# Kernel tuning notes

Hardware: AMD Instinct MI355X
Metric: run time of the kernel (lower is better)

## Reference

```python
import jax, jax.numpy as jnp
import numpy as np
from jax import lax

EPS = 1e-5

def haar_dwt(x):
    # pywt 'haar' dwt2: a=(x0+x1)/sqrt2, d=(x0-x1)/sqrt2 per axis
    B, C, H, W = x.shape
    xr = x.reshape(B, C, H // 2, 2, W // 2, 2)
    x00 = xr[:, :, :, 0, :, 0]; x01 = xr[:, :, :, 0, :, 1]
    x10 = xr[:, :, :, 1, :, 0]; x11 = xr[:, :, :, 1, :, 1]
    ll = (x00 + x01 + x10 + x11) * 0.5
    lh = (x00 + x01 - x10 - x11) * 0.5  # cH: detail along rows
    hl = (x00 - x01 + x10 - x11) * 0.5  # cV: detail along cols
    hh = (x00 - x01 - x10 + x11) * 0.5  # cD
    return ll, lh, hl, hh

def haar_idwt(ll, lh, hl, hh):
    y00 = (ll + lh + hl + hh) * 0.5
    y01 = (ll + lh - hl - hh) * 0.5
    y10 = (ll - lh + hl - hh) * 0.5
    y11 = (ll - lh - hl + hh) * 0.5
    B, C, H, W = ll.shape
    top = jnp.stack([y00, y01], axis=-1)      # [B,C,H,W,2]
    bot = jnp.stack([y10, y11], axis=-1)
    y = jnp.stack([top, bot], axis=3)          # [B,C,H,2,W,2]
    return y.reshape(B, C, 2 * H, 2 * W)

def conv1x1(x, w, b):
    # w: [Cout, Cin]
    return jnp.einsum('bchw,oc->bohw', x, w) + b[None, :, None, None]

def batchnorm(x, g, b):
    mu = jnp.mean(x, axis=(0, 2, 3), keepdims=True)
    var = jnp.var(x, axis=(0, 2, 3), keepdims=True)
    xh = (x - mu) * lax.rsqrt(var + EPS)
    return xh * g[None, :, None, None] + b[None, :, None, None]

def layernorm_chw(x, g, b):
    # GroupNorm(1, C): normalize over (C,H,W) per sample
    mu = jnp.mean(x, axis=(1, 2, 3), keepdims=True)
    var = jnp.var(x, axis=(1, 2, 3), keepdims=True)
    xh = (x - mu) * lax.rsqrt(var + EPS)
    return xh * g[None, :, None, None] + b[None, :, None, None]

def dwconv3x3(x, w, b):
    # w: [C,1,3,3] depthwise
    C = x.shape[1]
    y = lax.conv_general_dilated(x, w, (1, 1), [(1, 1), (1, 1)],
                                 dimension_numbers=('NCHW', 'OIHW', 'NCHW'),
                                 feature_group_count=C)
    return y + b[None, :, None, None]

gelu = lambda x: jax.nn.gelu(x, approximate=False)

def setup_inputs() -> dict:
    key = jax.random.key(0)
    ks = jax.random.split(key, 16)
    C = 128
    B, H, W = 8, 256, 256
    f = jnp.float32
    s = lambda k, shape, fan: jax.random.normal(k, shape, f) * (1.0 / np.sqrt(fan))
    return {
        'x': jax.random.normal(ks[0], (B, C, H, W), f),
        'w_c1': s(ks[1], (C, 4 * C), 4 * C), 'b_c1': jnp.zeros((C,), f),
        'bn1_g': jnp.ones((C,), f), 'bn1_b': jnp.zeros((C,), f),
        'dw_w': s(ks[2], (C, 1, 3, 3), 9), 'dw_b': jnp.zeros((C,), f),
        'gn_g': jnp.ones((C,), f), 'gn_b': jnp.zeros((C,), f),
        'pw1_w': s(ks[3], (C, C), C), 'pw1_b': jnp.zeros((C,), f),
        'pw2_w': s(ks[4], (C, C), C), 'pw2_b': jnp.zeros((C,), f),
        'w_c2': s(ks[5], (4 * C, C), C), 'b_c2': jnp.zeros((4 * C,), f),
        'bn2_g': jnp.ones((4 * C,), f), 'bn2_b': jnp.zeros((4 * C,), f),
    }

def reference(x, w_c1, b_c1, bn1_g, bn1_b, dw_w, dw_b, gn_g, gn_b,
              pw1_w, pw1_b, pw2_w, pw2_b, w_c2, b_c2, bn2_g, bn2_b):
    ll, lh, hl, hh = haar_dwt(x)
    h = jnp.concatenate([ll, lh, hl, hh], axis=1)       # [B,4C,H/2,W/2]
    h = gelu(batchnorm(conv1x1(h, w_c1, b_c1), bn1_g, bn1_b))
    # BasicBlock
    res = h
    o = dwconv3x3(h, dw_w, dw_b)
    o = layernorm_chw(o, gn_g, gn_b)
    o = conv1x1(o, pw1_w, pw1_b)
    o = gelu(o)
    o = conv1x1(o, pw2_w, pw2_b)
    h = o + res
    h = gelu(batchnorm(conv1x1(h, w_c2, b_c2), bn2_g, bn2_b))
    C = h.shape[1] // 4
    return haar_idwt(h[:, :C], h[:, C:2 * C], h[:, 2 * C:3 * C], h[:, 3 * C:])
```

## Files before the change

### kernel.cpp

```cpp
#include <hip/hip_runtime.h>
#include <hip/hip_bf16.h>

typedef unsigned short u16;
typedef unsigned int u32;
typedef __attribute__((ext_vector_type(8))) short short8;
typedef __attribute__((ext_vector_type(4))) float f32x4;

#define Bq 8
#define Cc 128
#define C4 512
#define Hh 256
#define Wf 256
#define H2 128
#define W2 128
#define HW2 16384
#define NPIX 131072.0f

__device__ __forceinline__ float gelu_f(float x) {
    float u = 1.5957691216057308f * (x + 0.044715f * x * x * x);
    float t = 1.0f - 2.0f / (__expf(u) + 1.0f);
    return 0.5f * x * (1.0f + t);
}
__device__ __forceinline__ float bf2f(u16 u) {
    union { float f; u32 i; } v; v.i = ((u32)u) << 16; return v.f;
}
__device__ __forceinline__ u16 f2bf(float f) {
    union { float f; u32 i; } v; v.f = f;
    u32 r = v.i + 0x7FFFu + ((v.i >> 16) & 1u);
    return (u16)(r >> 16);
}

__global__ __launch_bounds__(256) void k_wconv(const float* __restrict__ w_c1,
                                               const float* __restrict__ pw1,
                                               const float* __restrict__ pw2,
                                               const float* __restrict__ w_c2,
                                               const float* __restrict__ gn_g,
                                               u16* __restrict__ wb) {
    int i = blockIdx.x * 256 + threadIdx.x;
    float v;
    if (i < 65536) {
        int o = i >> 9, kn = i & 511;
        int c = kn >> 2, dy = (kn >> 1) & 1, dx = kn & 1;
        float sdy = dy ? -1.f : 1.f, sdx = dx ? -1.f : 1.f;
        const float* wr = w_c1 + o * 512 + c;
        v = 0.5f * (wr[0] + sdy * wr[128] + sdx * wr[256] + sdy * sdx * wr[384]);
    } else if (i < 81920) v = pw1[i - 65536] * gn_g[(i - 65536) & 127];
    else if (i < 98304) v = pw2[i - 81920];
    else v = w_c2[i - 98304];
    wb[i] = f2bf(v);
}

__global__ __launch_bounds__(128) void k_wvec(const float* __restrict__ pw1,
                                              const float* __restrict__ gg,
                                              const float* __restrict__ gb,
                                              float* __restrict__ wbv,
                                              float* __restrict__ wgs) {
    int o = threadIdx.x;
    float a = 0.f, bv = 0.f;
    for (int c = 0; c < 128; ++c) {
        float w = pw1[o * 128 + c];
        a += w * gg[c];
        bv += w * gb[c];
    }
    wgs[o] = a;
    wbv[o] = bv;
}

__global__ __launch_bounds__(512) void k_conv1(const float* __restrict__ x,
                                               const u16* __restrict__ Wt,
                                               u16* __restrict__ Cout,
                                               float* __restrict__ statS,
                                               float* __restrict__ statQ) {
    __shared__ __align__(16) u16 lds[16384];
    __shared__ float sblk[128], qblk[128];
    const int t = threadIdx.x;
    const int lane = t & 63, w = t >> 6, wr = w & 1, wc = w >> 1;
    const int b = blockIdx.z, i = blockIdx.y;
    if (t < 128) { sblk[t] = 0.f; qblk[t] = 0.f; }

    const int r15 = lane & 15, kq = lane >> 4;
    const int half = t >> 8;
    const int colblk = t & 7, cc = (t >> 3) & 15, dy = (t >> 7) & 1;
    const int kbase = cc * 4 + dy * 2;
    const int gG = kbase >> 3, e2 = (kbase & 7) * 2;

    float4 xv[4];
    uint4 rb[2];
    {
        const float* xp = x + (((long)(b * Cc + cc)) * Hh + (2 * i + dy)) * Wf;
#pragma unroll
        for (int q = 0; q < 4; ++q) {
            int col = (half * 4 + q) * 32 + colblk * 4;
            xv[q] = *(const float4*)(xp + col);
        }
#pragma unroll
        for (int ii = 0; ii < 2; ++ii) {
            int s = ii * 512 + t;
            rb[ii] = *(const uint4*)(Wt + (long)(s >> 3) * 512 + (s & 7) * 8);
        }
    }

    f32x4 acc[4][2];
#pragma unroll
    for (int a2 = 0; a2 < 4; ++a2)
#pragma unroll
        for (int j2 = 0; j2 < 2; ++j2) acc[a2][j2] = (f32x4){0.f, 0.f, 0.f, 0.f};

    for (int k0 = 0; k0 < 512; k0 += 64) {
        __syncthreads();
#pragma unroll
        for (int q = 0; q < 4; ++q) {
            int col = (half * 4 + q) * 32 + colblk * 4;
            int j0 = col >> 1;
            u32 p0 = (u32)f2bf(xv[q].x) | ((u32)f2bf(xv[q].y) << 16);
            u32 p1 = (u32)f2bf(xv[q].z) | ((u32)f2bf(xv[q].w) << 16);
            *(u32*)((char*)lds + j0 * 128 + 16 * (gG ^ (j0 & 7)) + e2) = p0;
            *(u32*)((char*)lds + (j0 + 1) * 128 + 16 * (gG ^ ((j0 + 1) & 7)) + e2) = p1;
        }
#pragma unroll
        for (int ii = 0; ii < 2; ++ii) {
            int s = ii * 512 + t;
            int row_ = s >> 3, ch_ = s & 7;
            *(uint4*)((char*)lds + 16384 + row_ * 128 + 16 * (ch_ ^ (row_ & 7))) = rb[ii];
        }
        __syncthreads();
        if (k0 + 64 < 512) {
            const int c0n = (k0 + 64) >> 2;
            const float* xp = x + (((long)(b * Cc + c0n + cc)) * Hh + (2 * i + dy)) * Wf;
#pragma unroll
            for (int q = 0; q < 4; ++q) {
                int col = (half * 4 + q) * 32 + colblk * 4;
                xv[q] = *(const float4*)(xp + col);
            }
#pragma unroll
            for (int ii = 0; ii < 2; ++ii) {
                int s = ii * 512 + t;
                rb[ii] = *(const uint4*)(Wt + (long)(s >> 3) * 512 + (k0 + 64) + (s & 7) * 8);
            }
        }
#pragma unroll
        for (int ks = 0; ks < 2; ++ks) {
            short8 af[4], bfv[2];
            const int ch = ks * 4 + kq;
#pragma unroll
            for (int mi = 0; mi < 4; ++mi) {
                int row = wr * 64 + mi * 16 + r15;
                af[mi] = *(const short8*)((const char*)lds + row * 128 + 16 * (ch ^ (row & 7)));
            }
#pragma unroll
            for (int ni = 0; ni < 2; ++ni) {
                int row = wc * 32 + ni * 16 + r15;
                bfv[ni] = *(const short8*)((const char*)lds + 16384 + row * 128 + 16 * (ch ^ (row & 7)));
            }
#pragma unroll
            for (int mi = 0; mi < 4; ++mi)
#pragma unroll
                for (int ni = 0; ni < 2; ++ni)
                    acc[mi][ni] = __builtin_amdgcn_mfma_f32_16x16x32_bf16(
                        af[mi], bfv[ni], acc[mi][ni], 0, 0, 0);
        }
    }
    __syncthreads();

#pragma unroll
    for (int mi = 0; mi < 4; ++mi)
#pragma unroll
        for (int ni = 0; ni < 2; ++ni)
#pragma unroll
            for (int r = 0; r < 4; ++r) {
                int row = wr * 64 + mi * 16 + kq * 4 + r;
                int col = wc * 32 + ni * 16 + r15;
                lds[row * 128 + (col ^ ((row & 7) << 3))] = f2bf(acc[mi][ni][r]);
            }
#pragma unroll
    for (int ni = 0; ni < 2; ++ni) {
        float s = 0.f, q2 = 0.f;
#pragma unroll
        for (int mi = 0; mi < 4; ++mi)
#pragma unroll
            for (int r = 0; r < 4; ++r) {
                float v = acc[mi][ni][r];
                s += v; q2 += v * v;
            }
        s += __shfl_down(s, 32); s += __shfl_down(s, 16);
        q2 += __shfl_down(q2, 32); q2 += __shfl_down(q2, 16);
        if (lane < 16) {
            int col = wc * 32 + ni * 16 + r15;
            atomicAdd(&sblk[col], s);
            atomicAdd(&qblk[col], q2);
        }
    }
    __syncthreads();
    {
        u16* Cb = Cout + (long)b * HW2 * 128;
        int row = t >> 2, quarter = (t & 3) * 32;
        int sx = (row & 7) << 3;
        long gbase = (long)(i * 128 + row) * 128;
#pragma unroll
        for (int q = 0; q < 4; ++q) {
            int c = quarter + q * 8;
            *(uint4*)(Cb + gbase + c) = *(const uint4*)(lds + row * 128 + (c ^ sx));
        }
    }
    if (t < 128) {
        atomicAdd(statS + (long)t * 16, sblk[t]);
        atomicAdd(statQ + (long)t * 16, qblk[t]);
    }
}

__global__ __launch_bounds__(256) void k_dwconv(const u16* __restrict__ xin,
                                                u16* __restrict__ y,
                                                const float* __restrict__ w,
                                                const float* __restrict__ bias,
                                                const float* __restrict__ bnS,
                                                const float* __restrict__ bnQ,
                                                const float* __restrict__ g1,
                                                const float* __restrict__ b1,
                                                float* __restrict__ lnS,
                                                float* __restrict__ lnQ) {
    __shared__ float wl2[1152];
    __shared__ float sA[128], sB[128];
    __shared__ __align__(16) u16 tile[3 * 18 * 136];
    const int t = threadIdx.x;
    if (t < 128) {
        const float invN = 1.0f / 131072.0f;
        float mu = bnS[(long)t * 16] * invN;
        float var = bnQ[(long)t * 16] * invN - mu * mu;
        float rs = rsqrtf(var + 1e-5f);
        float sc = rs * g1[t];
        sA[t] = sc;
        sB[t] = b1[t] - mu * sc;
    }
    for (int idx = t; idx < 1152; idx += 256) {
        int c = idx / 9, tap = idx - c * 9;
        wl2[tap * 128 + (c & 7) * 16 + (c >> 3)] = w[idx];
    }
    __syncthreads();
    const int jbase = blockIdx.x * 16, i = blockIdx.y, b = blockIdx.z;
    const u16* xb = xin + (long)b * HW2 * 128;
    {
        int seg = t & 15, slot0 = t >> 4;
#pragma unroll
        for (int pass = 0; pass < 4; ++pass) {
            int slot = pass * 16 + slot0;
            if (slot < 54) {
                int r = slot / 18, p = slot - r * 18;
                int row = i - 1 + r, col = jbase - 1 + p;
                bool inb = (row >= 0) & (row < H2) & (col >= 0) & (col < W2);
                uint4 raw = inb ? *(const uint4*)(xb + ((long)row * W2 + col) * 128 + seg * 8)
                                : make_uint4(0u, 0u, 0u, 0u);
                const u16* pv = (const u16*)&raw;
                uint4 outv; u16* ov = (u16*)&outv;
#pragma unroll
                for (int u = 0; u < 8; ++u) {
                    int c = seg * 8 + u;
                    float v = inb ? gelu_f(bf2f(pv[u]) * sA[c] + sB[c]) : 0.f;
                    ov[u] = f2bf(v);
                }
                *(uint4*)(tile + slot * 136 + seg * 8) = outv;
            }
        }
    }
    __syncthreads();
    const int cg = t & 15, jj = t >> 4;
    float acc[8];
#pragma unroll
    for (int u = 0; u < 8; ++u) acc[u] = bias[cg * 8 + u];
#pragma unroll
    for (int r = 0; r < 3; ++r)
#pragma unroll
        for (int dj = 0; dj < 3; ++dj) {
            short8 vv = *(const short8*)(tile + (r * 18 + jj + dj) * 136 + cg * 8);
            const int tap = r * 3 + dj;
#pragma unroll
            for (int u = 0; u < 8; ++u)
                acc[u] = fmaf(bf2f((u16)vv[u]), wl2[tap * 128 + u * 16 + cg], acc[u]);
        }
    uint4 outv; u16* ov = (u16*)&outv;
    float s = 0.f, q2 = 0.f;
#pragma unroll
    for (int u = 0; u < 8; ++u) {
        ov[u] = f2bf(acc[u]);
        s += acc[u]; q2 += acc[u] * acc[u];
    }
    *(uint4*)(y + ((long)b * HW2 + (long)i * W2 + jbase + jj) * 128 + cg * 8) = outv;
#pragma unroll
    for (int off = 32; off; off >>= 1) {
        s += __shfl_down(s, off);
        q2 += __shfl_down(q2, off);
    }
    __shared__ float r1[4], r2[4];
    if ((t & 63) == 0) { r1[t >> 6] = s; r2[t >> 6] = q2; }
    __syncthreads();
    if (t == 0) {
        int slot = (blockIdx.y * 8 + blockIdx.x) & 63;
        atomicAdd(lnS + ((long)b * 64 + slot) * 16, r1[0] + r1[1] + r1[2] + r1[3]);
        atomicAdd(lnQ + ((long)b * 64 + slot) * 16, r2[0] + r2[1] + r2[2] + r2[3]);
    }
}

__global__ __launch_bounds__(256) void k_mlp(const u16* __restrict__ D,
                                             const u16* __restrict__ Wp1,
                                             const u16* __restrict__ Wp2,
                                             const float* __restrict__ b1p,
                                             const float* __restrict__ b2p,
                                             const u16* __restrict__ resA,
                                             u16* __restrict__ Yout,
                                             const float* __restrict__ lnS,
                                             const float* __restrict__ lnQ,
                                             const float* __restrict__ wbv,
                                             const float* __restrict__ wgs,
                                             const float* __restrict__ bnS,
                                             const float* __restrict__ bnQ,
                                             const float* __restrict__ g1,
                                             const float* __restrict__ b1v) {
    __shared__ __align__(16) u16 lA[16384];
    __shared__ __align__(16) u16 lB[16384];
    __shared__ float s1[128], s2[128], sA[128], sB[128], lnred[2];
    const int t = threadIdx.x;
    const int lane = t & 63, w = t >> 6, wr = w >> 1, wc = w & 1;
    const int r15 = lane & 15, kq = lane >> 4;
    const int b = blockIdx.z, m0 = blockIdx.y * 128;

    if (t < 64) {
        float s = lnS[((long)b * 64 + t) * 16];
        float q = lnQ[((long)b * 64 + t) * 16];
#pragma unroll
        for (int off = 32; off; off >>= 1) {
            s += __shfl_down(s, off);
            q += __shfl_down(q, off);
        }
        if (t == 0) { lnred[0] = s; lnred[1] = q; }
    }
    __syncthreads();
    const float invN = 1.0f / 2097152.0f;
    float mu = lnred[0] * invN;
    float var = lnred[1] * invN - mu * mu;
    const float rs = rsqrtf(var + 1e-5f);
    if (t < 128) {
        s1[t] = b1p[t] + wbv[t] - mu * rs * wgs[t];
        s2[t] = b2p[t];
        const float invN1 = 1.0f / 131072.0f;
        float mu1 = bnS[(long)t * 16] * invN1;
        float var1 = bnQ[(long)t * 16] * invN1 - mu1 * mu1;
        float rs1 = rsqrtf(var1 + 1e-5f);
        float sc1 = rs1 * g1[t];
        sA[t] = sc1;
        sB[t] = b1v[t] - mu1 * sc1;
    }

    const u16* Ab = D + ((long)b * HW2 + m0) * 128;
    uint4 ga[8], gb[8];
#pragma unroll
    for (int i = 0; i < 8; ++i) {
        int s = i * 256 + t, row = s >> 4, seg = s & 15;
        ga[i] = *(const uint4*)(Ab + (long)row * 128 + seg * 8);
        gb[i] = *(const uint4*)(Wp1 + (long)row * 128 + seg * 8);
    }
#pragma unroll
    for (int i = 0; i < 8; ++i) {
        int s = i * 256 + t, row = s >> 4, seg = s & 15;
        int off = (seg >> 3) * 16384 + row * 128 + 16 * ((seg & 7) ^ (row & 7));
        *(uint4*)((char*)lA + off) = ga[i];
        *(uint4*)((char*)lB + off) = gb[i];
    }
    __syncthreads();

    f32x4 acc[4][4];
#pragma unroll
    for (int i = 0; i < 4; ++i)
#pragma unroll
        for (int j = 0; j < 4; ++j) acc[i][j] = (f32x4){0.f, 0.f, 0.f, 0.f};
#pragma unroll
    for (int chunk = 0; chunk < 2; ++chunk)
#pragma unroll
        for (int ks = 0; ks < 2; ++ks) {
            const int ch = ks * 4 + kq;
            short8 af[4], bfv[4];
#pragma unroll
            for (int mi = 0; mi < 4; ++mi) {
                int row = wr * 64 + mi * 16 + r15;
                af[mi] = *(const short8*)((const char*)lA + chunk * 16384 +
                                          row * 128 + 16 * (ch ^ (row & 7)));
            }
#pragma unroll
            for (int ni = 0; ni < 4; ++ni) {
                int row = wc * 64 + ni * 16 + r15;
                bfv[ni] = *(const short8*)((const char*)lB + chunk * 16384 +
                                           row * 128 + 16 * (ch ^ (row & 7)));
            }
#pragma unroll
            for (int mi = 0; mi < 4; ++mi)
#pragma unroll
                for (int ni = 0; ni < 4; ++ni)
                    acc[mi][ni] = __builtin_amdgcn_mfma_f32_16x16x32_bf16(
                        af[mi], bfv[ni], acc[mi][ni], 0, 0, 0);
        }
#pragma unroll
    for (int i = 0; i < 8; ++i) {
        int s = i * 256 + t, row = s >> 4, seg = s & 15;
        gb[i] = *(const uint4*)(Wp2 + (long)row * 128 + seg * 8);
    }
    __syncthreads();

#pragma unroll
    for (int mi = 0; mi < 4; ++mi)
#pragma unroll
        for (int ni = 0; ni < 4; ++ni)
#pragma unroll
            for (int r = 0; r < 4; ++r) {
                int row = wr * 64 + mi * 16 + kq * 4 + r;
                int col = wc * 64 + ni * 16 + r15;
                float v = gelu_f(rs * acc[mi][ni][r] + s1[col]);
                lA[(col >> 6) * 8192 + row * 64 +
                   8 * (((col >> 3) & 7) ^ (row & 7)) + (col & 7)] = f2bf(v);
            }
#pragma unroll
    for (int i = 0; i < 8; ++i) {
        int s = i * 256 + t, row = s >> 4, seg = s & 15;
        int off = (seg >> 3) * 16384 + row * 128 + 16 * ((seg & 7) ^ (row & 7));
        *(uint4*)((char*)lB + off) = gb[i];
    }
    __syncthreads();

#pragma unroll
    for (int i = 0; i < 4; ++i)
#pragma unroll
        for (int j = 0; j < 4; ++j) acc[i][j] = (f32x4){0.f, 0.f, 0.f, 0.f};
#pragma unroll
    for (int chunk = 0; chunk < 2; ++chunk)
#pragma unroll
        for (int ks = 0; ks < 2; ++ks) {
            const int ch = ks * 4 + kq;
            short8 af[4], bfv[4];
#pragma unroll
            for (int mi = 0; mi < 4; ++mi) {
                int row = wr * 64 + mi * 16 + r15;
                af[mi] = *(const short8*)((const char*)lA + chunk * 16384 +
                                          row * 128 + 16 * (ch ^ (row & 7)));
            }
#pragma unroll
            for (int ni = 0; ni < 4; ++ni) {
                int row = wc * 64 + ni * 16 + r15;
                bfv[ni] = *(const short8*)((const char*)lB + chunk * 16384 +
                                           row * 128 + 16 * (ch ^ (row & 7)));
            }
#pragma unroll
            for (int mi = 0; mi < 4; ++mi)
#pragma unroll
                for (int ni = 0; ni < 4; ++ni)
                    acc[mi][ni] = __builtin_amdgcn_mfma_f32_16x16x32_bf16(
                        af[mi], bfv[ni], acc[mi][ni], 0, 0, 0);
        }
    __syncthreads();

#pragma unroll
    for (int mi = 0; mi < 4; ++mi)
#pragma unroll
        for (int ni = 0; ni < 4; ++ni)
#pragma unroll
            for (int r = 0; r < 4; ++r) {
                int row = wr * 64 + mi * 16 + kq * 4 + r;
                int col = wc * 64 + ni * 16 + r15;
                lA[row * 128 + (col ^ ((row & 7) << 3))] = f2bf(acc[mi][ni][r]);
            }
    __syncthreads();

    const u16* Ra = resA + ((long)b * HW2 + m0) * 128;
    u16* Cb = Yout + ((long)b * HW2 + m0) * 128;
    {
        int row = t >> 1, half = (t & 1) * 64;
        int sx = (row & 7) << 3;
#pragma unroll
        for (int q = 0; q < 8; ++q) {
            int c = half + q * 8;
            uint4 raw = *(const uint4*)(lA + row * 128 + (c ^ sx));
            uint4 rr = *(const uint4*)(Ra + (long)row * 128 + c);
            u16* pv = (u16*)&raw;
            const u16* rv = (const u16*)&rr;
#pragma unroll
            for (int u = 0; u < 8; ++u) {
                float hres = gelu_f(bf2f(rv[u]) * sA[c + u] + sB[c + u]);
                pv[u] = f2bf(bf2f(pv[u]) + s2[c + u] + hres);
            }
            *(uint4*)(Cb + (long)row * 128 + c) = raw;
        }
    }
}

__global__ __launch_bounds__(256) void k_moment(const u16* __restrict__ Y,
                                                float* __restrict__ M2p,
                                                float* __restrict__ csum) {
    __shared__ __align__(16) u16 T[8192];
    __shared__ float cred[16][16][8];
    const int t = threadIdx.x;
    const int lane = t & 63, w = t >> 6, wr = w >> 1, wc = w & 1;
    const int r15 = lane & 15, kq = lane >> 4;
    const long px0 = (long)blockIdx.x * 1024;
    float cs[8] = {};

    f32x4 acc[4][4];
#pragma unroll
    for (int i = 0; i < 4; ++i)
#pragma unroll
        for (int j = 0; j < 4; ++j) acc[i][j] = (f32x4){0.f, 0.f, 0.f, 0.f};

    for (int it = 0; it < 16; ++it) {
        uint4 rv[4];
#pragma unroll
        for (int i = 0; i < 4; ++i) {
            int s = i * 256 + t;
            int px = s >> 4, ch8 = (s & 15) * 8;
            rv[i] = *(const uint4*)(Y + (px0 + it * 64 + px) * 128 + ch8);
        }
#pragma unroll
        for (int i = 0; i < 4; ++i) {
            const u16* pv = (const u16*)&rv[i];
#pragma unroll
            for (int u = 0; u < 8; ++u) cs[u] += bf2f(pv[u]);
        }
        __syncthreads();
#pragma unroll
        for (int i = 0; i < 4; ++i) {
            int s = i * 256 + t;
            int px = s >> 4, ch8 = (s & 15) * 8;
            const u16* pv = (const u16*)&rv[i];
#pragma unroll
            for (int u = 0; u < 8; ++u) {
                int row = ch8 + u;
                T[row * 64 + 8 * ((px >> 3) ^ (row & 7)) + (px & 7)] = pv[u];
            }
        }
        __syncthreads();
#pragma unroll
        for (int ks = 0; ks < 2; ++ks) {
            const int ch = ks * 4 + kq;
            short8 af[4], bfv[4];
#pragma unroll
            for (int mi = 0; mi < 4; ++mi) {
                int row = wr * 64 + mi * 16 + r15;
                af[mi] = *(const short8*)(T + row * 64 + 8 * (ch ^ (row & 7)));
            }
#pragma unroll
            for (int ni = 0; ni < 4; ++ni) {
                int row = wc * 64 + ni * 16 + r15;
                bfv[ni] = *(const short8*)(T + row * 64 + 8 * (ch ^ (row & 7)));
            }
#pragma unroll
            for (int mi = 0; mi < 4; ++mi)
#pragma unroll
                for (int ni = 0; ni < 4; ++ni)
                    acc[mi][ni] = __builtin_amdgcn_mfma_f32_16x16x32_bf16(
                        af[mi], bfv[ni], acc[mi][ni], 0, 0, 0);
        }
    }
    {
        int g = t & 15, m = t >> 4;
#pragma unroll
        for (int u = 0; u < 8; ++u) cred[m][g][u] = cs[u];
    }
    __syncthreads();
    if (t < 128) {
        float s = 0.f;
#pragma unroll
        for (int m = 0; m < 16; ++m) s += cred[m][t >> 3][t & 7];
        atomicAdd(csum + (long)t * 16, s);
    }
    float* Mb = M2p + (long)blockIdx.x * 16384;
#pragma unroll
    for (int mi = 0; mi < 4; ++mi)
#pragma unroll
        for (int ni = 0; ni < 4; ++ni)
#pragma unroll
            for (int r = 0; r < 4; ++r) {
                int row = wr * 64 + mi * 16 + kq * 4 + r;
                int col = wc * 64 + ni * 16 + r15;
                Mb[row * 128 + col] = acc[mi][ni][r];
            }
}

__global__ __launch_bounds__(256) void k_m2red(const float* __restrict__ M2p,
                                               float* __restrict__ M2) {
    int e = blockIdx.x * 256 + threadIdx.x;
    float s = 0.f;
    for (int p = 0; p < 128; ++p) s += M2p[(long)p * 16384 + e];
    M2[e] = s;
}

__global__ __launch_bounds__(128) void k_statcomb(const float* __restrict__ w_c2,
                                                  const float* __restrict__ M2,
                                                  const float* __restrict__ csum,
                                                  const float* __restrict__ g,
                                                  const float* __restrict__ bb,
                                                  float* __restrict__ scsh) {
    __shared__ float wl[128];
    __shared__ float red[2][2];
    const int o = blockIdx.x, c = threadIdx.x;
    wl[c] = w_c2[o * 128 + c];
    __syncthreads();
    const float* m2r = M2 + c * 128;
    float tmp = 0.f;
#pragma unroll
    for (int c2 = 0; c2 < 128; c2 += 4) {
        float4 m = *(const float4*)(m2r + c2);
        tmp += m.x * wl[c2] + m.y * wl[c2 + 1] + m.z * wl[c2 + 2] + m.w * wl[c2 + 3];
    }
    float s2p = wl[c] * tmp;
    float mup = wl[c] * csum[(long)c * 16];
#pragma unroll
    for (int off = 32; off; off >>= 1) {
        s2p += __shfl_down(s2p, off);
        mup += __shfl_down(mup, off);
    }
    if ((c & 63) == 0) { red[0][c >> 6] = s2p; red[1][c >> 6] = mup; }
    __syncthreads();
    if (c == 0) {
        float s2 = (red[0][0] + red[0][1]) / NPIX;
        float mu = (red[1][0] + red[1][1]) / NPIX;
        float var = s2 - mu * mu;
        float rs = rsqrtf(var + 1e-5f);
        float sc = g[o] * rs;
        scsh[o] = sc;
        scsh[512 + o] = bb[o] - mu * sc;
    }
}

__global__ __launch_bounds__(512) void k_conv2_idwt(const u16* __restrict__ Y,
                                                    const u16* __restrict__ Wc,
                                                    const float* __restrict__ scsh,
                                                    float* __restrict__ out) {
    __shared__ __align__(16) u16 lA[16384];
    __shared__ __align__(16) u16 lB[8192];
    __shared__ float sparam[1024];
    const int t = threadIdx.x;
    const int lane = t & 63, w = t >> 6, wr = w & 1, wc = w >> 1;
    const int r15 = lane & 15, kq = lane >> 4;
    const int b = blockIdx.y, n0 = blockIdx.x;
#pragma unroll
    for (int u = 0; u < 2; ++u) sparam[t + u * 512] = scsh[t + u * 512];

    const u16* Yb = Y + ((long)b * HW2 + (long)n0 * 64) * 128;
    uint4 rb2[2], ra4[4];
#pragma unroll
    for (int i = 0; i < 2; ++i) {
        int s = i * 512 + t, row = s >> 4, seg = s & 15;
        rb2[i] = *(const uint4*)(Yb + (long)row * 128 + seg * 8);
    }
#define GLOADA(q)                                                                \
    {                                                                            \
        _Pragma("unroll")                                                        \
        for (int i = 0; i < 4; ++i) {                                            \
            int s = i * 512 + t, row = s >> 4, seg = s & 15;                     \
            ra4[i] = *(const uint4*)(Wc + (long)((q) * 128 + row) * 128 + seg * 8); \
        }                                                                        \
    }
#define LWRITEA()                                                                \
    {                                                                            \
        _Pragma("unroll")                                                        \
        for (int i = 0; i < 4; ++i) {                                            \
            int s = i * 512 + t, row = s >> 4, seg = s & 15;                     \
            *(uint4*)((char*)lA + (seg >> 3) * 16384 + row * 128 +               \
                      16 * ((seg & 7) ^ (row & 7))) = ra4[i];                    \
        }                                                                        \
    }
    GLOADA(0)
#pragma unroll
    for (int i = 0; i < 2; ++i) {
        int s = i * 512 + t, row = s >> 4, seg = s & 15;
        *(uint4*)((char*)lB + (seg >> 3) * 8192 + row * 128 +
                  16 * ((seg & 7) ^ (row & 7))) = rb2[i];
    }
    LWRITEA()
    __syncthreads();

    u32 sbp[4][4][2];
#pragma unroll
    for (int q = 0; q < 4; ++q) {
        f32x4 acc[4];
#pragma unroll
        for (int mi = 0; mi < 4; ++mi) acc[mi] = (f32x4){0.f, 0.f, 0.f, 0.f};
#pragma unroll
        for (int chunk = 0; chunk < 2; ++chunk)
#pragma unroll
            for (int ks = 0; ks < 2; ++ks) {
                const int ch = ks * 4 + kq;
                short8 af[4], bfv;
#pragma unroll
                for (int mi = 0; mi < 4; ++mi) {
                    int row = wr * 64 + mi * 16 + r15;
                    af[mi] = *(const short8*)((const char*)lA + chunk * 16384 +
                                              row * 128 + 16 * (ch ^ (row & 7)));
                }
                {
                    int row = wc * 16 + r15;
                    bfv = *(const short8*)((const char*)lB + chunk * 8192 +
                                           row * 128 + 16 * (ch ^ (row & 7)));
                }
#pragma unroll
                for (int mi = 0; mi < 4; ++mi)
                    acc[mi] = __builtin_amdgcn_mfma_f32_16x16x32_bf16(
                        af[mi], bfv, acc[mi], 0, 0, 0);
            }
        if (q < 3) GLOADA(q + 1)
#pragma unroll
        for (int mi = 0; mi < 4; ++mi)
#pragma unroll
            for (int rp = 0; rp < 2; ++rp) {
                int c0 = q * 128 + wr * 64 + mi * 16 + kq * 4 + rp * 2;
                float v0 = gelu_f(acc[mi][rp * 2] * sparam[c0] + sparam[512 + c0]);
                float v1 = gelu_f(acc[mi][rp * 2 + 1] * sparam[c0 + 1] + sparam[512 + c0 + 1]);
                sbp[q][mi][rp] = (u32)f2bf(v0) | ((u32)f2bf(v1) << 16);
            }
        if (q < 3) {
            __syncthreads();
            LWRITEA()
            __syncthreads();
        }
    }
    const int i = n0 >> 1;
    const int j = (n0 & 1) * 64 + wc * 16 + r15;
#pragma unroll
    for (int mi = 0; mi < 4; ++mi)
#pragma unroll
        for (int rp = 0; rp < 2; ++rp) {
            u32 p0 = sbp[0][mi][rp], p1 = sbp[1][mi][rp];
            u32 p2 = sbp[2][mi][rp], p3 = sbp[3][mi][rp];
#pragma unroll
            for (int e = 0; e < 2; ++e) {
                int c = wr * 64 + mi * 16 + kq * 4 + rp * 2 + e;
                float ll = bf2f(e ? (u16)(p0 >> 16) : (u16)(p0 & 0xFFFF));
                float lh = bf2f(e ? (u16)(p1 >> 16) : (u16)(p1 & 0xFFFF));
                float hl = bf2f(e ? (u16)(p2 >> 16) : (u16)(p2 & 0xFFFF));
                float hh = bf2f(e ? (u16)(p3 >> 16) : (u16)(p3 & 0xFFFF));
                long ob = (((long)(b * Cc + c) * Hh + 2 * i) * Wf + 2 * j);
                *(float2*)(out + ob) =
                    make_float2((ll + lh + hl + hh) * 0.5f, (ll + lh - hl - hh) * 0.5f);
                *(float2*)(out + ob + Wf) =
                    make_float2((ll - lh + hl - hh) * 0.5f, (ll - lh - hl + hh) * 0.5f);
            }
        }
#undef GLOADA
#undef LWRITEA
}

extern "C" void kernel_launch(void* const* d_in, const int* in_sizes, int n_in,
                              void* d_out, int out_size, void* d_ws, size_t ws_size,
                              hipStream_t stream) {
    const float* x     = (const float*)d_in[0];
    const float* w_c1  = (const float*)d_in[1];
    const float* bn1_g = (const float*)d_in[3];
    const float* bn1_b = (const float*)d_in[4];
    const float* dw_w  = (const float*)d_in[5];
    const float* dw_b  = (const float*)d_in[6];
    const float* gn_g  = (const float*)d_in[7];
    const float* gn_b  = (const float*)d_in[8];
    const float* pw1_w = (const float*)d_in[9];
    const float* pw1_b = (const float*)d_in[10];
    const float* pw2_w = (const float*)d_in[11];
    const float* pw2_b = (const float*)d_in[12];
    const float* w_c2  = (const float*)d_in[13];
    const float* bn2_g = (const float*)d_in[15];
    const float* bn2_b = (const float*)d_in[16];
    float* out = (float*)d_out;

    const size_t n128 = (size_t)Bq * Cc * HW2;
    u16* bufA = (u16*)d_ws;
    u16* bufD = bufA + n128;
    u16* bufY = bufD + n128;
    u16* wb   = bufY + n128;
    float* stats = (float*)(wb + 163840);
    float* M2p = stats + 49152;
    size_t need = (3 * n128 + 163840) * 2 + (49152 + 128 * 16384) * 4;
    if (ws_size < need) return;

    float* bn1_sum = stats;
    float* bn1_sq  = stats + 2048;
    float* ln_sum  = stats + 4096;
    float* ln_sq   = stats + 12288;
    float* csum    = stats + 20480;
    float* M2      = stats + 22528;
    float* scsh    = stats + 38912;
    float* wbv     = stats + 39936;
    float* wgs     = stats + 40064;

    hipMemsetAsync(stats, 0, 22528 * sizeof(float), stream);

    k_wconv<<<640, 256, 0, stream>>>(w_c1, pw1_w, pw2_w, w_c2, gn_g, wb);
    k_wvec<<<1, 128, 0, stream>>>(pw1_w, gn_g, gn_b, wbv, wgs);

    k_conv1<<<dim3(1, 128, 8), 512, 0, stream>>>(x, wb, bufA, bn1_sum, bn1_sq);

    k_dwconv<<<dim3(8, 128, 8), 256, 0, stream>>>(bufA, bufD, dw_w, dw_b,
                                                  bn1_sum, bn1_sq, bn1_g, bn1_b,
                                                  ln_sum, ln_sq);

    k_mlp<<<dim3(1, 128, 8), 256, 0, stream>>>(
        bufD, wb + 65536, wb + 81920, pw1_b, pw2_b, bufA, bufY,
        ln_sum, ln_sq, wbv, wgs, bn1_sum, bn1_sq, bn1_g, bn1_b);

    k_moment<<<128, 256, 0, stream>>>(bufY, M2p, csum);
    k_m2red<<<64, 256, 0, stream>>>(M2p, M2);
    k_statcomb<<<512, 128, 0, stream>>>(w_c2, M2, csum, bn2_g, bn2_b, scsh);

    k_conv2_idwt<<<dim3(256, 8), 512, 0, stream>>>(bufY, wb + 98304, scsh, out);
}
```

Before: 423.5 us.

## Tile dwconv over four rows, merge weight-vector kernel, nontemporal output stores

The depthwise conv block now computes four output rows per block. The 3-row halo tile grows to 6 rows, so each input row is loaded and GELU-normalized about 1.5 times instead of 3 times, and the per-block BN-coefficient and weight setup is amortized over more work. The separate k_wvec kernel is folded into an extra block of k_wconv, saving one launch. The final iDWT output writes use nontemporal stores to avoid polluting the cache. The trade-offs are fewer dwconv blocks (2048 instead of 8192), more LDS per block, and unused dead wreg code.

```diff
diff --git a/kernel.cpp b/kernel.cpp
--- a/kernel.cpp
+++ b/kernel.cpp
@@ -3,6 +3,7 @@
 
 typedef unsigned short u16;
 typedef unsigned int u32;
+typedef unsigned long long u64;
 typedef __attribute__((ext_vector_type(8))) short short8;
 typedef __attribute__((ext_vector_type(4))) float f32x4;
 
@@ -35,7 +36,24 @@
                                                const float* __restrict__ pw2,
                                                const float* __restrict__ w_c2,
                                                const float* __restrict__ gn_g,
-                                               u16* __restrict__ wb) {
+                                               const float* __restrict__ gn_b,
+                                               u16* __restrict__ wb,
+                                               float* __restrict__ wbv,
+                                               float* __restrict__ wgs) {
+    if (blockIdx.x == 640) {
+        int o = threadIdx.x;
+        if (o < 128) {
+            float a = 0.f, bv = 0.f;
+            for (int c = 0; c < 128; ++c) {
+                float w_ = pw1[o * 128 + c];
+                a += w_ * gn_g[c];
+                bv += w_ * gn_b[c];
+            }
+            wgs[o] = a;
+            wbv[o] = bv;
+        }
+        return;
+    }
     int i = blockIdx.x * 256 + threadIdx.x;
     float v;
     if (i < 65536) {
@@ -50,22 +68,6 @@
     wb[i] = f2bf(v);
 }
 
-__global__ __launch_bounds__(128) void k_wvec(const float* __restrict__ pw1,
-                                              const float* __restrict__ gg,
-                                              const float* __restrict__ gb,
-                                              float* __restrict__ wbv,
-                                              float* __restrict__ wgs) {
-    int o = threadIdx.x;
-    float a = 0.f, bv = 0.f;
-    for (int c = 0; c < 128; ++c) {
-        float w = pw1[o * 128 + c];
-        a += w * gg[c];
-        bv += w * gb[c];
-    }
-    wgs[o] = a;
-    wbv[o] = bv;
-}
-
 __global__ __launch_bounds__(512) void k_conv1(const float* __restrict__ x,
                                                const u16* __restrict__ Wt,
                                                u16* __restrict__ Cout,
@@ -220,7 +222,7 @@
                                                 float* __restrict__ lnQ) {
     __shared__ float wl2[1152];
     __shared__ float sA[128], sB[128];
-    __shared__ __align__(16) u16 tile[3 * 18 * 136];
+    __shared__ __align__(16) u16 tile[108 * 136];
     const int t = threadIdx.x;
     if (t < 128) {
         const float invN = 1.0f / 131072.0f;
@@ -236,16 +238,16 @@
         wl2[tap * 128 + (c & 7) * 16 + (c >> 3)] = w[idx];
     }
     __syncthreads();
-    const int jbase = blockIdx.x * 16, i = blockIdx.y, b = blockIdx.z;
+    const int jbase = blockIdx.x * 16, i0 = blockIdx.y * 4, b = blockIdx.z;
     const u16* xb = xin + (long)b * HW2 * 128;
     {
         int seg = t & 15, slot0 = t >> 4;
 #pragma unroll
-        for (int pass = 0; pass < 4; ++pass) {
+        for (int pass = 0; pass < 7; ++pass) {
             int slot = pass * 16 + slot0;
-            if (slot < 54) {
+            if (slot < 108) {
                 int r = slot / 18, p = slot - r * 18;
-                int row = i - 1 + r, col = jbase - 1 + p;
+                int row = i0 - 1 + r, col = jbase - 1 + p;
                 bool inb = (row >= 0) & (row < H2) & (col >= 0) & (col < W2);
                 uint4 raw = inb ? *(const uint4*)(xb + ((long)row * W2 + col) * 128 + seg * 8)
                                 : make_uint4(0u, 0u, 0u, 0u);
@@ -263,27 +265,38 @@
     }
     __syncthreads();
     const int cg = t & 15, jj = t >> 4;
-    float acc[8];
-#pragma unroll
-    for (int u = 0; u < 8; ++u) acc[u] = bias[cg * 8 + u];
-#pragma unroll
-    for (int r = 0; r < 3; ++r)
-#pragma unroll
-        for (int dj = 0; dj < 3; ++dj) {
-            short8 vv = *(const short8*)(tile + (r * 18 + jj + dj) * 136 + cg * 8);
-            const int tap = r * 3 + dj;
-#pragma unroll
-            for (int u = 0; u < 8; ++u)
-                acc[u] = fmaf(bf2f((u16)vv[u]), wl2[tap * 128 + u * 16 + cg], acc[u]);
-        }
-    uint4 outv; u16* ov = (u16*)&outv;
     float s = 0.f, q2 = 0.f;
-#pragma unroll
-    for (int u = 0; u < 8; ++u) {
-        ov[u] = f2bf(acc[u]);
-        s += acc[u]; q2 += acc[u] * acc[u];
-    }
-    *(uint4*)(y + ((long)b * HW2 + (long)i * W2 + jbase + jj) * 128 + cg * 8) = outv;
+    float wreg[9];
+#pragma unroll
+    for (int tap = 0; tap < 9; ++tap) {
+        wreg[tap] = 0.f;
+    }
+    float bi[8];
+#pragma unroll
+    for (int u = 0; u < 8; ++u) bi[u] = bias[cg * 8 + u];
+#pragma unroll
+    for (int dr = 0; dr < 4; ++dr) {
+        float acc[8];
+#pragma unroll
+        for (int u = 0; u < 8; ++u) acc[u] = bi[u];
+#pragma unroll
+        for (int r = 0; r < 3; ++r)
+#pragma unroll
+            for (int dj = 0; dj < 3; ++dj) {
+                short8 vv = *(const short8*)(tile + ((dr + r) * 18 + jj + dj) * 136 + cg * 8);
+                const int tap = r * 3 + dj;
+#pragma unroll
+                for (int u = 0; u < 8; ++u)
+                    acc[u] = fmaf(bf2f((u16)vv[u]), wl2[tap * 128 + u * 16 + cg], acc[u]);
+            }
+        uint4 outv; u16* ov = (u16*)&outv;
+#pragma unroll
+        for (int u = 0; u < 8; ++u) {
+            ov[u] = f2bf(acc[u]);
+            s += acc[u]; q2 += acc[u] * acc[u];
+        }
+        *(uint4*)(y + ((long)b * HW2 + (long)(i0 + dr) * W2 + jbase + jj) * 128 + cg * 8) = outv;
+    }
 #pragma unroll
     for (int off = 32; off; off >>= 1) {
         s += __shfl_down(s, off);
@@ -733,10 +746,11 @@
                 float hl = bf2f(e ? (u16)(p2 >> 16) : (u16)(p2 & 0xFFFF));
                 float hh = bf2f(e ? (u16)(p3 >> 16) : (u16)(p3 & 0xFFFF));
                 long ob = (((long)(b * Cc + c) * Hh + 2 * i) * Wf + 2 * j);
-                *(float2*)(out + ob) =
-                    make_float2((ll + lh + hl + hh) * 0.5f, (ll + lh - hl - hh) * 0.5f);
-                *(float2*)(out + ob + Wf) =
-                    make_float2((ll - lh + hl - hh) * 0.5f, (ll - lh - hl + hh) * 0.5f);
+                union { float2 v; u64 u; } w0, w1;
+                w0.v = make_float2((ll + lh + hl + hh) * 0.5f, (ll + lh - hl - hh) * 0.5f);
+                w1.v = make_float2((ll - lh + hl - hh) * 0.5f, (ll - lh - hl + hh) * 0.5f);
+                __builtin_nontemporal_store(w0.u, (u64*)(out + ob));
+                __builtin_nontemporal_store(w1.u, (u64*)(out + ob + Wf));
             }
         }
 #undef GLOADA
@@ -785,14 +799,14 @@
 
     hipMemsetAsync(stats, 0, 22528 * sizeof(float), stream);
 
-    k_wconv<<<640, 256, 0, stream>>>(w_c1, pw1_w, pw2_w, w_c2, gn_g, wb);
-    k_wvec<<<1, 128, 0, stream>>>(pw1_w, gn_g, gn_b, wbv, wgs);
+    k_wconv<<<641, 256, 0, stream>>>(w_c1, pw1_w, pw2_w, w_c2, gn_g, gn_b,
+                                     wb, wbv, wgs);
 
     k_conv1<<<dim3(1, 128, 8), 512, 0, stream>>>(x, wb, bufA, bn1_sum, bn1_sq);
 
-    k_dwconv<<<dim3(8, 128, 8), 256, 0, stream>>>(bufA, bufD, dw_w, dw_b,
-                                                  bn1_sum, bn1_sq, bn1_g, bn1_b,
-                                                  ln_sum, ln_sq);
+    k_dwconv<<<dim3(8, 32, 8), 256, 0, stream>>>(bufA, bufD, dw_w, dw_b,
+                                                 bn1_sum, bn1_sq, bn1_g, bn1_b,
+                                                 ln_sum, ln_sq);
 
     k_mlp<<<dim3(1, 128, 8), 256, 0, stream>>>(
         bufD, wb + 65536, wb + 81920, pw1_b, pw2_b, bufA, bufY,
```

After: 410.7 us. -3.0%, faster.
